# Kernel optimization log

Hardware: AMD Instinct MI355X
Metric: run time of the kernel (lower is better)

The kernel has to match this reference:

```python
import jax, jax.numpy as jnp
import numpy as np
from jax import lax

B, H, W = 256, 28, 28
LATENT = 64
SOM = (16, 16)
FLAT = 7 * 7 * 256  # encoder feature size after two 2x2 pools


def conv2d_same(x, w, b):
    # x: NHWC, w: HWIO
    return lax.conv_general_dilated(x, w, (1, 1), 'SAME',
                                    dimension_numbers=('NHWC', 'HWIO', 'NHWC')) + b


def maxpool_2x2(x):
    return lax.reduce_window(x, -jnp.inf, lax.max, (1, 2, 2, 1), (1, 2, 2, 1), 'SAME')


def upsample_2x(x):
    return jnp.repeat(jnp.repeat(x, 2, axis=1), 2, axis=2)


def encode(x, conv1_w, conv1_b, conv2_w, conv2_b, enc_w, enc_b):
    h = jax.nn.relu(conv2d_same(x, conv1_w, conv1_b))      # [B,28,28,256]
    h = maxpool_2x2(h)                                      # [B,14,14,256]
    h = jax.nn.relu(conv2d_same(h, conv2_w, conv2_b))      # [B,14,14,256]
    h = maxpool_2x2(h)                                      # [B,7,7,256]
    h = h.reshape(h.shape[0], -1)                           # [B,12544]
    return h @ enc_w + enc_b                                # [B,latent]


def decode(z, dec_w, dec_b, deconv1_w, deconv1_b, deconv2_w, deconv2_b):
    h = z @ dec_w + dec_b                                   # [B,12544]
    h = h.reshape(-1, 7, 7, 256)
    h = upsample_2x(h)                                      # [B,14,14,256]
    h = jax.nn.relu(conv2d_same(h, deconv1_w, deconv1_b))
    h = upsample_2x(h)                                      # [B,28,28,256]
    h = conv2d_same(h, deconv2_w, deconv2_b)                # [B,28,28,1]
    return jax.nn.sigmoid(h)


def setup_inputs() -> dict:
    key = jax.random.key(0)
    ks = jax.random.split(key, 12)
    tn = lambda k, shp, s: jax.random.truncated_normal(k, -2.0, 2.0, shp, jnp.float32) * s
    return {
        'x': jax.random.uniform(ks[0], (B, H, W, 1), jnp.float32),
        'conv1_w': tn(ks[1], (4, 4, 1, 256), 0.1),
        'conv1_b': jnp.full((256,), 0.1, jnp.float32),
        'conv2_w': tn(ks[2], (4, 4, 256, 256), 0.1),
        'conv2_b': jnp.full((256,), 0.1, jnp.float32),
        'enc_w': tn(ks[3], (FLAT, LATENT), 0.02),
        'enc_b': jnp.zeros((LATENT,), jnp.float32),
        'embeddings': tn(ks[4], (SOM[0], SOM[1], LATENT), 0.05),
        'dec_w': tn(ks[5], (LATENT, FLAT), 0.02),
        'dec_b': jnp.zeros((FLAT,), jnp.float32),
        'deconv1_w': tn(ks[6], (4, 4, 256, 256), 0.1),
        'deconv1_b': jnp.full((256,), 0.1, jnp.float32),
        'deconv2_w': tn(ks[7], (4, 4, 256, 1), 0.1),
        'deconv2_b': jnp.full((1,), 0.1, jnp.float32),
    }


def reference(x, conv1_w, conv1_b, conv2_w, conv2_b, enc_w, enc_b, embeddings,
              dec_w, dec_b, deconv1_w, deconv1_b, deconv2_w, deconv2_b):
    z_e = encode(x, conv1_w, conv1_b, conv2_w, conv2_b, enc_w, enc_b)  # [B,D]
    emb_flat = embeddings.reshape(-1, LATENT)                          # [K,D]
    # squared euclidean distances [B,K] (cdist pattern)
    z_dist_flat = jnp.sum(jnp.square(z_e[:, None, :] - emb_flat[None, :, :]), axis=-1)
    k = jnp.argmin(z_dist_flat, axis=-1)                               # [B]
    z_q = emb_flat[k]                                                  # [B,D]
    x_hat_e = decode(z_e, dec_w, dec_b, deconv1_w, deconv1_b, deconv2_w, deconv2_b)
    x_hat_q = decode(z_q, dec_w, dec_b, deconv1_w, deconv1_b, deconv2_w, deconv2_b)
    return jnp.stack([x_hat_e, x_hat_q], axis=0)  # [2,B,28,28,1]
```

## Files before the change

### kernel.cpp

```cpp
#include <hip/hip_runtime.h>
#include <hip/hip_bf16.h>

typedef unsigned short u16;
using short8 = __attribute__((ext_vector_type(8))) short;
using half8  = __attribute__((ext_vector_type(8))) _Float16;
using half4  = __attribute__((ext_vector_type(4))) _Float16;
using half2v = __attribute__((ext_vector_type(2))) _Float16;
using f32x4  = __attribute__((ext_vector_type(4))) float;

__device__ __forceinline__ u16 f2bf(float f) {
    unsigned int u = __float_as_uint(f);
    u += 0x7FFFu + ((u >> 16) & 1u);
    return (u16)(u >> 16);
}
__device__ __forceinline__ float bf2f(u16 h) {
    return __uint_as_float(((unsigned int)h) << 16);
}

__device__ __forceinline__ void gl_lds16(const void* g, void* l) {
    __builtin_amdgcn_global_load_lds((const __attribute__((address_space(1))) void*)g,
                                     (__attribute__((address_space(3))) void*)l, 16, 0, 0);
}

__global__ __launch_bounds__(256) void wprep_split_kernel(const float* __restrict__ src,
                                                          u16* __restrict__ hi, u16* __restrict__ lo) {
    int idx = blockIdx.x * 256 + threadIdx.x;
    int ci = idx & 255, n = (idx >> 8) & 255, kk = idx >> 16;
    float v = src[(kk * 256 + ci) * 256 + n];
    u16 h = f2bf(v);
    hi[idx] = h;
    lo[idx] = f2bf(v - bf2f(h));
}

__global__ __launch_bounds__(256) void wprep_f16_kernel(const float* __restrict__ src,
                                                        _Float16* __restrict__ dst) {
    int idx = blockIdx.x * 256 + threadIdx.x;
    int ci = idx & 255, n = (idx >> 8) & 255, kk = idx >> 16;
    dst[idx] = (_Float16)src[(kk * 256 + ci) * 256 + n];
}

__global__ __launch_bounds__(256) void wprep_c2_kernel(const float* __restrict__ src, _Float16* __restrict__ dst) {
    int idx = blockIdx.x * 256 + threadIdx.x;
    dst[idx] = (_Float16)src[idx];
}

__global__ __launch_bounds__(256) void conv1_pool_kernel(const float* __restrict__ x,
                                                         const float* __restrict__ w,
                                                         const float* __restrict__ bias,
                                                         u16* __restrict__ hi, u16* __restrict__ lo) {
    __shared__ float xs[5][5];
    const int blk = blockIdx.x;
    const int px = blk % 14, py = (blk / 14) % 14, b = blk / 196;
    const int t = threadIdx.x;
    if (t < 25) {
        int r = t / 5, c = t % 5;
        int gy = 2 * py - 1 + r, gx = 2 * px - 1 + c;
        xs[r][c] = (gy >= 0 && gy < 28 && gx >= 0 && gx < 28) ? x[(b * 28 + gy) * 28 + gx] : 0.f;
    }
    __syncthreads();
    float wr[16];
#pragma unroll
    for (int k = 0; k < 16; ++k) wr[k] = w[k * 256 + t];
    const float bs = bias[t];
    float m = -1e30f;
#pragma unroll
    for (int dy = 0; dy < 2; ++dy)
#pragma unroll
        for (int dx = 0; dx < 2; ++dx) {
            float acc = bs;
#pragma unroll
            for (int ky = 0; ky < 4; ++ky)
#pragma unroll
                for (int kx = 0; kx < 4; ++kx)
                    acc += xs[dy + ky][dx + kx] * wr[ky * 4 + kx];
            m = fmaxf(m, acc);
        }
    m = fmaxf(m, 0.f);
    u16 h = f2bf(m);
    int o = blk * 256 + t;
    hi[o] = h;
    lo[o] = f2bf(m - bf2f(h));
}

__global__ __launch_bounds__(256, 2) void conv2_split_v2(const u16* __restrict__ Ih, const u16* __restrict__ Il,
                                                         const u16* __restrict__ Wh, const u16* __restrict__ Wl,
                                                         const u16* __restrict__ zg,
                                                         const float* __restrict__ bias, float* __restrict__ out) {
    __shared__ __align__(16) short lds[32768];
    const int AL = 8192, BH = 16384, BL = 24576;
    const int t = threadIdx.x, lane = t & 63, w = t >> 6;
    const int wm = w >> 1, wn = w & 1;
    const int l16 = lane & 15, l4 = lane >> 4;
    const int m0 = blockIdx.x * 128, n0 = blockIdx.y * 128;
    const int rl = lane >> 3;
    const int chS = (((lane & 7) ^ rl)) << 3;
    int ay[4], ax[4], ab[4], wb[4], aoff[4];
    bool av[4];
#pragma unroll
    for (int j = 0; j < 4; ++j) {
        const int r = w * 32 + j * 8 + rl;
        const int gm = m0 + r;
        const int b = gm / 196, rem = gm % 196;
        ay[j] = rem / 14; ax[j] = rem % 14; ab[j] = b * 196;
        wb[j] = (n0 + r) << 8;
    }
    f32x4 acc[4][4] = {};

    for (int kt = 0; kt < 64; ++kt) {
        const int kk = kt >> 2;
        if ((kt & 3) == 0) {
            const int ky = kk >> 2, kx = kk & 3;
#pragma unroll
            for (int j = 0; j < 4; ++j) {
                const int iy = ay[j] + ky - 1, ix = ax[j] + kx - 1;
                av[j] = ((unsigned)iy < 14u) && ((unsigned)ix < 14u);
                aoff[j] = (ab[j] + iy * 14 + ix) << 8;
            }
        }
        const int kc = (kt & 3) << 6;
        __syncthreads();
#pragma unroll
        for (int j = 0; j < 4; ++j) {
            const int rowb = (w * 32 + j * 8) << 6;
            const u16* gh = av[j] ? (Ih + aoff[j] + kc + chS) : zg;
            const u16* gl = av[j] ? (Il + aoff[j] + kc + chS) : zg;
            gl_lds16(gh, lds + rowb);
            gl_lds16(gl, lds + AL + rowb);
            const int woff = (kk << 16) + wb[j] + kc + chS;
            gl_lds16(Wh + woff, lds + BH + rowb);
            gl_lds16(Wl + woff, lds + BL + rowb);
        }
        __syncthreads();
#pragma unroll
        for (int ks = 0; ks < 2; ++ks) {
            short8 bhf[4], blf[4];
#pragma unroll
            for (int ni = 0; ni < 4; ++ni) {
                const int row = wn * 64 + ni * 16 + l16;
                const int p = (ks * 4 + l4) ^ (row & 7);
                const int off = (row << 6) + (p << 3);
                bhf[ni] = *(const short8*)&lds[BH + off];
                blf[ni] = *(const short8*)&lds[BL + off];
            }
#pragma unroll
            for (int mi = 0; mi < 4; ++mi) {
                const int row = wm * 64 + mi * 16 + l16;
                const int p = (ks * 4 + l4) ^ (row & 7);
                const int off = (row << 6) + (p << 3);
                const short8 ah = *(const short8*)&lds[off];
                const short8 al = *(const short8*)&lds[AL + off];
#pragma unroll
                for (int ni = 0; ni < 4; ++ni) {
                    acc[mi][ni] = __builtin_amdgcn_mfma_f32_16x16x32_bf16(ah, bhf[ni], acc[mi][ni], 0, 0, 0);
                    acc[mi][ni] = __builtin_amdgcn_mfma_f32_16x16x32_bf16(ah, blf[ni], acc[mi][ni], 0, 0, 0);
                    acc[mi][ni] = __builtin_amdgcn_mfma_f32_16x16x32_bf16(al, bhf[ni], acc[mi][ni], 0, 0, 0);
                }
            }
        }
    }
#pragma unroll
    for (int ni = 0; ni < 4; ++ni) {
        const int col = n0 + wn * 64 + ni * 16 + l16;
        const float bv = bias[col];
#pragma unroll
        for (int mi = 0; mi < 4; ++mi) {
            const int mrow = m0 + wm * 64 + mi * 16 + l4 * 4;
#pragma unroll
            for (int r = 0; r < 4; ++r)
                out[(size_t)(mrow + r) * 256 + col] = fmaxf(acc[mi][ni][r] + bv, 0.f);
        }
    }
}

__global__ __launch_bounds__(256, 3) void deconv1_f16_v2(const _Float16* __restrict__ I,
                                                         const _Float16* __restrict__ WT,
                                                         const _Float16* __restrict__ zg,
                                                         const float* __restrict__ bias,
                                                         _Float16* __restrict__ out) {
    __shared__ __align__(16) _Float16 lds[16384];
    const int BO = 8192;
    const int t = threadIdx.x, lane = t & 63, w = t >> 6;
    const int wm = w >> 1, wn = w & 1;
    const int l16 = lane & 15, l4 = lane >> 4;
    const int m0 = blockIdx.x * 128, n0 = blockIdx.y * 128;
    const int rl = lane >> 3;
    const int chS = (((lane & 7) ^ rl)) << 3;
    int ay[4], ax[4], ab[4], wb[4], aoff[4];
    bool av[4];
#pragma unroll
    for (int j = 0; j < 4; ++j) {
        const int r = w * 32 + j * 8 + rl;
        const int gm = m0 + r;
        const int b = gm / 196, rem = gm % 196;
        ay[j] = rem / 14; ax[j] = rem % 14; ab[j] = b * 49;
        wb[j] = (n0 + r) << 8;
    }
    f32x4 acc[4][4] = {};

    for (int kt = 0; kt < 64; ++kt) {
        const int kk = kt >> 2;
        if ((kt & 3) == 0) {
            const int ky = kk >> 2, kx = kk & 3;
#pragma unroll
            for (int j = 0; j < 4; ++j) {
                const int iy = ay[j] + ky - 1, ix = ax[j] + kx - 1;
                av[j] = ((unsigned)iy < 14u) && ((unsigned)ix < 14u);
                aoff[j] = (ab[j] + (iy >> 1) * 7 + (ix >> 1)) << 8;
            }
        }
        const int kc = (kt & 3) << 6;
        __syncthreads();
#pragma unroll
        for (int j = 0; j < 4; ++j) {
            const int rowb = (w * 32 + j * 8) << 6;
            const _Float16* ga = av[j] ? (I + aoff[j] + kc + chS) : zg;
            gl_lds16(ga, lds + rowb);
            gl_lds16(WT + (kk << 16) + wb[j] + kc + chS, lds + BO + rowb);
        }
        __syncthreads();
#pragma unroll
        for (int ks = 0; ks < 2; ++ks) {
            half8 bf[4];
#pragma unroll
            for (int ni = 0; ni < 4; ++ni) {
                const int row = wn * 64 + ni * 16 + l16;
                const int p = (ks * 4 + l4) ^ (row & 7);
                bf[ni] = *(const half8*)&lds[BO + (row << 6) + (p << 3)];
            }
#pragma unroll
            for (int mi = 0; mi < 4; ++mi) {
                const int row = wm * 64 + mi * 16 + l16;
                const int p = (ks * 4 + l4) ^ (row & 7);
                const half8 af = *(const half8*)&lds[(row << 6) + (p << 3)];
#pragma unroll
                for (int ni = 0; ni < 4; ++ni)
                    acc[mi][ni] = __builtin_amdgcn_mfma_f32_16x16x32_f16(af, bf[ni], acc[mi][ni], 0, 0, 0);
            }
        }
    }
#pragma unroll
    for (int ni = 0; ni < 4; ++ni) {
        const int col = n0 + wn * 64 + ni * 16 + l16;
        const float bv = bias[col];
#pragma unroll
        for (int mi = 0; mi < 4; ++mi) {
            const int mrow = m0 + wm * 64 + mi * 16 + l4 * 4;
#pragma unroll
            for (int r = 0; r < 4; ++r)
                out[(size_t)(mrow + r) * 256 + col] = (_Float16)fmaxf(acc[mi][ni][r] + bv, 0.f);
        }
    }
}

__global__ __launch_bounds__(256) void pool2_kernel(const float* __restrict__ h2, float* __restrict__ h2p) {
    int idx = blockIdx.x * 256 + threadIdx.x;
    int c = idx & 255;
    int rest = idx >> 8;
    int px = rest % 7, py = (rest / 7) % 7, b = rest / 49;
    const float* base = h2 + (((size_t)(b * 14 + 2 * py)) * 14 + 2 * px) * 256 + c;
    float v = fmaxf(fmaxf(base[0], base[256]), fmaxf(base[14 * 256], base[14 * 256 + 256]));
    h2p[idx] = v;
}

__global__ __launch_bounds__(256) void enc_kernel(const float* __restrict__ h2p, const float* __restrict__ ew,
                                                  const float* __restrict__ eb, float* __restrict__ zcat) {
    __shared__ float arow[12544];
    __shared__ float part[256];
    const int b = blockIdx.x, t = threadIdx.x;
    const float* src = h2p + (size_t)b * 12544;
    for (int i = t; i < 12544; i += 256) arow[i] = src[i];
    __syncthreads();
    const int n = t & 63, chunk = t >> 6;
    float acc = 0.f;
    const int k0 = chunk * 3136;
    for (int k = k0; k < k0 + 3136; ++k) acc += arow[k] * ew[k * 64 + n];
    part[t] = acc;
    __syncthreads();
    if (t < 64) zcat[b * 64 + t] = part[t] + part[t + 64] + part[t + 128] + part[t + 192] + eb[t];
}

__global__ __launch_bounds__(256) void som_kernel(const float* __restrict__ emb, float* __restrict__ zcat) {
    __shared__ float zrow[64];
    __shared__ float sd[256];
    __shared__ int si[256];
    const int b = blockIdx.x, t = threadIdx.x;
    if (t < 64) zrow[t] = zcat[b * 64 + t];
    __syncthreads();
    float acc = 0.f;
    const float* e = emb + t * 64;
    for (int d = 0; d < 64; ++d) { float df = zrow[d] - e[d]; acc += df * df; }
    sd[t] = acc; si[t] = t;
    __syncthreads();
    for (int off = 128; off >= 1; off >>= 1) {
        if (t < off) {
            float d2 = sd[t + off]; int i2 = si[t + off];
            if (d2 < sd[t] || (d2 == sd[t] && i2 < si[t])) { sd[t] = d2; si[t] = i2; }
        }
        __syncthreads();
    }
    const int k = si[0];
    if (t < 64) zcat[(256 + b) * 64 + t] = emb[k * 64 + t];
}

__global__ __launch_bounds__(256) void dec_kernel(const float* __restrict__ zcat, const float* __restrict__ dw,
                                                  const float* __restrict__ db, _Float16* __restrict__ dech) {
    __shared__ float z[8][64];
    const int t = threadIdx.x;
    const int bg = blockIdx.x / 49;
    const int nc = blockIdx.x % 49;
    for (int i = t; i < 512; i += 256) z[i >> 6][i & 63] = zcat[bg * 512 + i];
    __syncthreads();
    const int n = nc * 256 + t;
    const float bv = db[n];
    float acc[8];
#pragma unroll
    for (int j = 0; j < 8; ++j) acc[j] = bv;
    for (int k = 0; k < 64; ++k) {
        float wv = dw[(size_t)k * 12544 + n];
#pragma unroll
        for (int j = 0; j < 8; ++j) acc[j] += z[j][k] * wv;
    }
#pragma unroll
    for (int j = 0; j < 8; ++j) dech[((size_t)(bg * 8 + j)) * 12544 + n] = (_Float16)acc[j];
}

__global__ __launch_bounds__(256) void deconv2_v2(const _Float16* __restrict__ d1, const _Float16* __restrict__ w,
                                                  const float* __restrict__ bias, float* __restrict__ out) {
    __shared__ _Float16 ds[6400];
    __shared__ _Float16 wl[4096];
    const int t = threadIdx.x;
    const int blk = blockIdx.x;
    const int tile = blk % 49, b = blk / 49;
    const int ty = tile / 7, tx = tile % 7;
    const int iy0 = 2 * ty - 1, ix0 = 2 * tx - 1;
    for (int i = t; i < 1024; i += 256)
        *(half4*)&wl[i * 4] = *(const half4*)&w[i * 4];
    const half4 z4 = {};
    for (int i = t; i < 1600; i += 256) {
        const int pix = i >> 6, c4 = (i & 63) << 2;
        const int py = pix / 5, px = pix % 5;
        const int iy = iy0 + py, ix = ix0 + px;
        half4 v = z4;
        if ((unsigned)iy < 14u && (unsigned)ix < 14u)
            v = *(const half4*)&d1[(((size_t)(b * 14 + iy)) * 14 + ix) * 256 + c4];
        *(half4*)&ds[pix * 256 + c4] = v;
    }
    __syncthreads();
    const int wv = t >> 6, lane = t & 63;
    const int ci0 = lane * 4;
    const float bv = bias[0];
#pragma unroll
    for (int pp = 0; pp < 4; ++pp) {
        const int p = wv + pp * 4;
        const int oy = ty * 4 + (p >> 2), ox = tx * 4 + (p & 3);
        float acc = 0.f;
#pragma unroll
        for (int kk = 0; kk < 16; ++kk) {
            const int ky = kk >> 2, kx = kk & 3;
            const int iy = oy + ky - 1, ix = ox + kx - 1;
            if ((unsigned)iy < 28u && (unsigned)ix < 28u) {
                const int lp = ((iy >> 1) - iy0) * 5 + ((ix >> 1) - ix0);
                const half4 dv = *(const half4*)&ds[lp * 256 + ci0];
                const half4 wv4 = *(const half4*)&wl[kk * 256 + ci0];
                half2v dlo = {dv.x, dv.y}, dhi = {dv.z, dv.w};
                half2v wlo = {wv4.x, wv4.y}, whi = {wv4.z, wv4.w};
                acc = __builtin_amdgcn_fdot2(dlo, wlo, acc, false);
                acc = __builtin_amdgcn_fdot2(dhi, whi, acc, false);
            }
        }
#pragma unroll
        for (int off = 32; off; off >>= 1) acc += __shfl_xor(acc, off);
        if (lane == 0) out[(size_t)b * 784 + oy * 28 + ox] = 1.f / (1.f + expf(-(acc + bv)));
    }
}

extern "C" void kernel_launch(void* const* d_in, const int* in_sizes, int n_in,
                              void* d_out, int out_size, void* d_ws, size_t ws_size,
                              hipStream_t stream) {
    const float* x    = (const float*)d_in[0];
    const float* c1w  = (const float*)d_in[1];
    const float* c1b  = (const float*)d_in[2];
    const float* c2w  = (const float*)d_in[3];
    const float* c2b  = (const float*)d_in[4];
    const float* ew   = (const float*)d_in[5];
    const float* eb   = (const float*)d_in[6];
    const float* emb  = (const float*)d_in[7];
    const float* dw   = (const float*)d_in[8];
    const float* db   = (const float*)d_in[9];
    const float* dc1w = (const float*)d_in[10];
    const float* dc1b = (const float*)d_in[11];
    const float* dc2w = (const float*)d_in[12];
    const float* dc2b = (const float*)d_in[13];
    float* out = (float*)d_out;

    char* ws = (char*)d_ws;
    size_t off = 0;
    auto alloc = [&](size_t bytes) { size_t o = off; off += (bytes + 255) & ~(size_t)255; return o; };

    u16*      h1p_hi = (u16*)(ws + alloc((size_t)256 * 196 * 256 * 2));
    u16*      h1p_lo = (u16*)(ws + alloc((size_t)256 * 196 * 256 * 2));
    u16*      w2T_hi = (u16*)(ws + alloc((size_t)16 * 256 * 256 * 2));
    u16*      w2T_lo = (u16*)(ws + alloc((size_t)16 * 256 * 256 * 2));
    float*    h2     = (float*)(ws + alloc((size_t)256 * 196 * 256 * 4));
    float*    h2p    = (float*)(ws + alloc((size_t)256 * 49 * 256 * 4));
    float*    zcat   = (float*)(ws + alloc((size_t)512 * 64 * 4));
    _Float16* dech   = (_Float16*)(ws + alloc((size_t)512 * 49 * 256 * 2));
    _Float16* dw1T   = (_Float16*)(ws + alloc((size_t)16 * 256 * 256 * 2));
    _Float16* d1     = (_Float16*)(ws + alloc((size_t)512 * 196 * 256 * 2));
    _Float16* w2h    = (_Float16*)(ws + alloc((size_t)4096 * 2));
    u16*      zg     = (u16*)(ws + alloc(256));

    hipMemsetAsync(zg, 0, 256, stream);
    wprep_split_kernel<<<4096, 256, 0, stream>>>(c2w, w2T_hi, w2T_lo);
    wprep_f16_kernel<<<4096, 256, 0, stream>>>(dc1w, dw1T);
    wprep_c2_kernel<<<16, 256, 0, stream>>>(dc2w, w2h);
    conv1_pool_kernel<<<50176, 256, 0, stream>>>(x, c1w, c1b, h1p_hi, h1p_lo);
    conv2_split_v2<<<dim3(392, 2), 256, 0, stream>>>(h1p_hi, h1p_lo, w2T_hi, w2T_lo, zg, c2b, h2);
    pool2_kernel<<<12544, 256, 0, stream>>>(h2, h2p);
    enc_kernel<<<256, 256, 0, stream>>>(h2p, ew, eb, zcat);
    som_kernel<<<256, 256, 0, stream>>>(emb, zcat);
    dec_kernel<<<3136, 256, 0, stream>>>(zcat, dw, db, dech);
    deconv1_f16_v2<<<dim3(784, 2), 256, 0, stream>>>(dech, dw1T, (const _Float16*)zg, dc1b, d1);
    deconv2_v2<<<25088, 256, 0, stream>>>(d1, w2h, dc2b, out);
}
```

Before: 891.3 us.

## Polyphase-decompose deconvs, double-buffer conv2 loads, and row-tile conv1

Both deconvolutions that follow nearest-neighbour upsampling are rewritten in polyphase form. The 4x4 taps that read the same source pixel are pre-summed into 9/6/6/4 effective taps per output parity, so deconv1 runs a smaller GEMM directly on the 7x7 input and deconv2 drops to 9 taps per pixel. conv2 gets a double-buffered LDS pipeline using vmcnt waits so global-to-LDS loads overlap the MFMAs. conv1 now handles a whole pooled row per block to cut block count and redundant input loads. Pre-summing the weights in fp16 slightly changes rounding, and the manual waitcnt pipelining depends on the load counts being right.

After: 841.0 us. 1.06x faster.

```diff
diff --git a/kernel.cpp b/kernel.cpp
--- a/kernel.cpp
+++ b/kernel.cpp
@@ -21,6 +21,10 @@
     __builtin_amdgcn_global_load_lds((const __attribute__((address_space(1))) void*)g,
                                      (__attribute__((address_space(3))) void*)l, 16, 0, 0);
 }
+
+#define PIPE_WAIT8() asm volatile("s_waitcnt vmcnt(8)" ::: "memory")
+#define PIPE_WAIT0() asm volatile("s_waitcnt vmcnt(0)" ::: "memory")
+#define BAR() __builtin_amdgcn_s_barrier()
 
 __global__ __launch_bounds__(256) void wprep_split_kernel(const float* __restrict__ src,
                                                           u16* __restrict__ hi, u16* __restrict__ lo) {
@@ -32,132 +36,178 @@
     lo[idx] = f2bf(v - bf2f(h));
 }
 
-__global__ __launch_bounds__(256) void wprep_f16_kernel(const float* __restrict__ src,
-                                                        _Float16* __restrict__ dst) {
-    int idx = blockIdx.x * 256 + threadIdx.x;
-    int ci = idx & 255, n = (idx >> 8) & 255, kk = idx >> 16;
-    dst[idx] = (_Float16)src[(kk * 256 + ci) * 256 + n];
-}
-
-__global__ __launch_bounds__(256) void wprep_c2_kernel(const float* __restrict__ src, _Float16* __restrict__ dst) {
-    int idx = blockIdx.x * 256 + threadIdx.x;
-    dst[idx] = (_Float16)src[idx];
-}
-
-__global__ __launch_bounds__(256) void conv1_pool_kernel(const float* __restrict__ x,
-                                                         const float* __restrict__ w,
-                                                         const float* __restrict__ bias,
-                                                         u16* __restrict__ hi, u16* __restrict__ lo) {
-    __shared__ float xs[5][5];
+__global__ __launch_bounds__(256) void wprep_dc1_par(const float* __restrict__ src, _Float16* __restrict__ dst) {
+    const int idx = blockIdx.x * 256 + threadIdx.x;
+    const int ci = idx & 255, n = (idx >> 8) & 255, tg = idx >> 16;
+    int p, j;
+    if (tg < 9)       { p = 0; j = tg; }
+    else if (tg < 15) { p = 1; j = tg - 9; }
+    else if (tg < 21) { p = 2; j = tg - 15; }
+    else              { p = 3; j = tg - 21; }
+    const int dy = p >> 1, dx = p & 1;
+    const int nx = 3 - dx;
+    const int oyi = j / nx, oxi = j % nx;
+    int ky0, kyn, kx0, kxn;
+    if (dy == 0) { ky0 = (oyi == 0) ? 0 : (oyi == 1 ? 1 : 3); kyn = (oyi == 1) ? 2 : 1; }
+    else         { ky0 = (oyi == 0) ? 0 : 2;                  kyn = 2; }
+    if (dx == 0) { kx0 = (oxi == 0) ? 0 : (oxi == 1 ? 1 : 3); kxn = (oxi == 1) ? 2 : 1; }
+    else         { kx0 = (oxi == 0) ? 0 : 2;                  kxn = 2; }
+    float s = 0.f;
+    for (int a = 0; a < kyn; ++a)
+        for (int c = 0; c < kxn; ++c)
+            s += src[(((ky0 + a) * 4 + (kx0 + c)) * 256 + ci) * 256 + n];
+    dst[((size_t)tg << 16) + (n << 8) + ci] = (_Float16)s;
+}
+
+__global__ __launch_bounds__(256) void wprep_dc2_par(const float* __restrict__ src, _Float16* __restrict__ dst) {
+    const int idx = blockIdx.x * 256 + threadIdx.x;
+    if (idx >= 9216) return;
+    const int ci = idx & 255;
+    const int j9 = (idx >> 8) % 9, p = (idx >> 8) / 9;
+    const int dy = p >> 1, dx = p & 1;
+    const int oyi = j9 / 3, oxi = j9 % 3;
+    float s = 0.f;
+    if (!((dy == 1 && oyi == 2) || (dx == 1 && oxi == 2))) {
+        int ky0, kyn, kx0, kxn;
+        if (dy == 0) { ky0 = (oyi == 0) ? 0 : (oyi == 1 ? 1 : 3); kyn = (oyi == 1) ? 2 : 1; }
+        else         { ky0 = (oyi == 0) ? 0 : 2;                  kyn = 2; }
+        if (dx == 0) { kx0 = (oxi == 0) ? 0 : (oxi == 1 ? 1 : 3); kxn = (oxi == 1) ? 2 : 1; }
+        else         { kx0 = (oxi == 0) ? 0 : 2;                  kxn = 2; }
+        for (int a = 0; a < kyn; ++a)
+            for (int c = 0; c < kxn; ++c)
+                s += src[((ky0 + a) * 4 + (kx0 + c)) * 256 + ci];
+    }
+    dst[idx] = (_Float16)s;
+}
+
+__global__ __launch_bounds__(256) void conv1_pool_v2(const float* __restrict__ x,
+                                                     const float* __restrict__ w,
+                                                     const float* __restrict__ bias,
+                                                     u16* __restrict__ hi, u16* __restrict__ lo) {
+    __shared__ float xs[5][32];
     const int blk = blockIdx.x;
-    const int px = blk % 14, py = (blk / 14) % 14, b = blk / 196;
+    const int py = blk % 14, b = blk / 14;
     const int t = threadIdx.x;
-    if (t < 25) {
-        int r = t / 5, c = t % 5;
-        int gy = 2 * py - 1 + r, gx = 2 * px - 1 + c;
-        xs[r][c] = (gy >= 0 && gy < 28 && gx >= 0 && gx < 28) ? x[(b * 28 + gy) * 28 + gx] : 0.f;
+    for (int i = t; i < 160; i += 256) {
+        const int r = i >> 5, c = i & 31;
+        const int gy = 2 * py - 1 + r, gx = c - 1;
+        float v = 0.f;
+        if ((unsigned)gy < 28u && (unsigned)gx < 28u) v = x[(b * 28 + gy) * 28 + gx];
+        xs[r][c] = v;
     }
     __syncthreads();
     float wr[16];
 #pragma unroll
     for (int k = 0; k < 16; ++k) wr[k] = w[k * 256 + t];
     const float bs = bias[t];
-    float m = -1e30f;
-#pragma unroll
-    for (int dy = 0; dy < 2; ++dy)
-#pragma unroll
-        for (int dx = 0; dx < 2; ++dx) {
-            float acc = bs;
-#pragma unroll
-            for (int ky = 0; ky < 4; ++ky)
-#pragma unroll
-                for (int kx = 0; kx < 4; ++kx)
-                    acc += xs[dy + ky][dx + kx] * wr[ky * 4 + kx];
-            m = fmaxf(m, acc);
-        }
-    m = fmaxf(m, 0.f);
-    u16 h = f2bf(m);
-    int o = blk * 256 + t;
-    hi[o] = h;
-    lo[o] = f2bf(m - bf2f(h));
-}
-
-__global__ __launch_bounds__(256, 2) void conv2_split_v2(const u16* __restrict__ Ih, const u16* __restrict__ Il,
+    for (int px = 0; px < 14; ++px) {
+        float m = 0.f;
+#pragma unroll
+        for (int dy = 0; dy < 2; ++dy)
+#pragma unroll
+            for (int dx = 0; dx < 2; ++dx) {
+                float a = bs;
+#pragma unroll
+                for (int ky = 0; ky < 4; ++ky)
+#pragma unroll
+                    for (int kx = 0; kx < 4; ++kx)
+                        a += xs[dy + ky][2 * px + dx + kx] * wr[ky * 4 + kx];
+                m = fmaxf(m, a);
+            }
+        u16 h = f2bf(m);
+        const int o = ((b * 14 + py) * 14 + px) * 256 + t;
+        hi[o] = h;
+        lo[o] = f2bf(m - bf2f(h));
+    }
+}
+
+__global__ __launch_bounds__(256, 2) void conv2_split_v3(const u16* __restrict__ Ih, const u16* __restrict__ Il,
                                                          const u16* __restrict__ Wh, const u16* __restrict__ Wl,
                                                          const u16* __restrict__ zg,
                                                          const float* __restrict__ bias, float* __restrict__ out) {
     __shared__ __align__(16) short lds[32768];
-    const int AL = 8192, BH = 16384, BL = 24576;
     const int t = threadIdx.x, lane = t & 63, w = t >> 6;
     const int wm = w >> 1, wn = w & 1;
     const int l16 = lane & 15, l4 = lane >> 4;
     const int m0 = blockIdx.x * 128, n0 = blockIdx.y * 128;
-    const int rl = lane >> 3;
-    const int chS = (((lane & 7) ^ rl)) << 3;
-    int ay[4], ax[4], ab[4], wb[4], aoff[4];
-    bool av[4];
+
+    const int rl8 = lane >> 3;
+    const int g = (lane & 7) ^ rl8;
+    const u16* selA = (g < 4 ? Ih : Il) + ((g & 3) << 3);
+    const u16* selB = (g < 4 ? Wh : Wl) + ((g & 3) << 3);
+
+    int ay[4], ax[4], ab[4], wb[4];
 #pragma unroll
     for (int j = 0; j < 4; ++j) {
-        const int r = w * 32 + j * 8 + rl;
+        const int r = w * 32 + j * 8 + rl8;
         const int gm = m0 + r;
         const int b = gm / 196, rem = gm % 196;
         ay[j] = rem / 14; ax[j] = rem % 14; ab[j] = b * 196;
         wb[j] = (n0 + r) << 8;
     }
+    int aoff[4]; bool av[4];
+    auto dectap = [&](int kk) {
+        const int ky = kk >> 2, kx = kk & 3;
+#pragma unroll
+        for (int j = 0; j < 4; ++j) {
+            const int iy = ay[j] + ky - 1, ix = ax[j] + kx - 1;
+            av[j] = ((unsigned)iy < 14u) && ((unsigned)ix < 14u);
+            aoff[j] = (ab[j] + iy * 14 + ix) << 8;
+        }
+    };
+    int rdA[4], rdB[4];
+#pragma unroll
+    for (int mi = 0; mi < 4; ++mi) {
+        const int ra = wm * 64 + mi * 16 + l16;
+        rdA[mi] = (ra << 6) + ((l4 ^ (ra & 7)) << 3);
+    }
+#pragma unroll
+    for (int ni = 0; ni < 4; ++ni) {
+        const int rb = wn * 64 + ni * 16 + l16;
+        rdB[ni] = 8192 + (rb << 6) + ((l4 ^ (rb & 7)) << 3);
+    }
+    auto stage = [&](int h) {
+        const int kk = h >> 3, kc = (h & 7) << 5;
+        const int buf = (h & 1) << 14;
+#pragma unroll
+        for (int j = 0; j < 4; ++j) {
+            const int rowb = buf + ((w * 32 + j * 8) << 6);
+            const u16* asrc = av[j] ? (selA + aoff[j] + kc) : zg;
+            gl_lds16(asrc, lds + rowb);
+            gl_lds16(selB + (kk << 16) + wb[j] + kc, lds + 8192 + rowb);
+        }
+    };
+
     f32x4 acc[4][4] = {};
-
-    for (int kt = 0; kt < 64; ++kt) {
-        const int kk = kt >> 2;
-        if ((kt & 3) == 0) {
-            const int ky = kk >> 2, kx = kk & 3;
-#pragma unroll
-            for (int j = 0; j < 4; ++j) {
-                const int iy = ay[j] + ky - 1, ix = ax[j] + kx - 1;
-                av[j] = ((unsigned)iy < 14u) && ((unsigned)ix < 14u);
-                aoff[j] = (ab[j] + iy * 14 + ix) << 8;
+    dectap(0);
+    stage(0);
+    for (int h = 0; h < 128; ++h) {
+        const int hn = (h < 127) ? h + 1 : 127;
+        if ((hn & 7) == 0) dectap(hn >> 3);
+        stage(hn);
+        PIPE_WAIT8();
+        BAR();
+        const int base = (h & 1) << 14;
+        short8 bh8[4], bl8[4];
+#pragma unroll
+        for (int ni = 0; ni < 4; ++ni) {
+            bh8[ni] = *(const short8*)&lds[base + rdB[ni]];
+            bl8[ni] = *(const short8*)&lds[base + (rdB[ni] ^ 32)];
+        }
+#pragma unroll
+        for (int mi = 0; mi < 4; ++mi) {
+            const short8 ah = *(const short8*)&lds[base + rdA[mi]];
+            const short8 al = *(const short8*)&lds[base + (rdA[mi] ^ 32)];
+#pragma unroll
+            for (int ni = 0; ni < 4; ++ni) {
+                acc[mi][ni] = __builtin_amdgcn_mfma_f32_16x16x32_bf16(ah, bh8[ni], acc[mi][ni], 0, 0, 0);
+                acc[mi][ni] = __builtin_amdgcn_mfma_f32_16x16x32_bf16(ah, bl8[ni], acc[mi][ni], 0, 0, 0);
+                acc[mi][ni] = __builtin_amdgcn_mfma_f32_16x16x32_bf16(al, bh8[ni], acc[mi][ni], 0, 0, 0);
             }
         }
-        const int kc = (kt & 3) << 6;
-        __syncthreads();
-#pragma unroll
-        for (int j = 0; j < 4; ++j) {
-            const int rowb = (w * 32 + j * 8) << 6;
-            const u16* gh = av[j] ? (Ih + aoff[j] + kc + chS) : zg;
-            const u16* gl = av[j] ? (Il + aoff[j] + kc + chS) : zg;
-            gl_lds16(gh, lds + rowb);
-            gl_lds16(gl, lds + AL + rowb);
-            const int woff = (kk << 16) + wb[j] + kc + chS;
-            gl_lds16(Wh + woff, lds + BH + rowb);
-            gl_lds16(Wl + woff, lds + BL + rowb);
-        }
-        __syncthreads();
-#pragma unroll
-        for (int ks = 0; ks < 2; ++ks) {
-            short8 bhf[4], blf[4];
-#pragma unroll
-            for (int ni = 0; ni < 4; ++ni) {
-                const int row = wn * 64 + ni * 16 + l16;
-                const int p = (ks * 4 + l4) ^ (row & 7);
-                const int off = (row << 6) + (p << 3);
-                bhf[ni] = *(const short8*)&lds[BH + off];
-                blf[ni] = *(const short8*)&lds[BL + off];
-            }
-#pragma unroll
-            for (int mi = 0; mi < 4; ++mi) {
-                const int row = wm * 64 + mi * 16 + l16;
-                const int p = (ks * 4 + l4) ^ (row & 7);
-                const int off = (row << 6) + (p << 3);
-                const short8 ah = *(const short8*)&lds[off];
-                const short8 al = *(const short8*)&lds[AL + off];
-#pragma unroll
-                for (int ni = 0; ni < 4; ++ni) {
-                    acc[mi][ni] = __builtin_amdgcn_mfma_f32_16x16x32_bf16(ah, bhf[ni], acc[mi][ni], 0, 0, 0);
-                    acc[mi][ni] = __builtin_amdgcn_mfma_f32_16x16x32_bf16(ah, blf[ni], acc[mi][ni], 0, 0, 0);
-                    acc[mi][ni] = __builtin_amdgcn_mfma_f32_16x16x32_bf16(al, bhf[ni], acc[mi][ni], 0, 0, 0);
-                }
-            }
-        }
-    }
+        BAR();
+    }
+    PIPE_WAIT0();
 #pragma unroll
     for (int ni = 0; ni < 4; ++ni) {
         const int col = n0 + wn * 64 + ni * 16 + l16;
@@ -172,82 +222,112 @@
     }
 }
 
-__global__ __launch_bounds__(256, 3) void deconv1_f16_v2(const _Float16* __restrict__ I,
-                                                         const _Float16* __restrict__ WT,
-                                                         const _Float16* __restrict__ zg,
-                                                         const float* __restrict__ bias,
-                                                         _Float16* __restrict__ out) {
-    __shared__ __align__(16) _Float16 lds[16384];
-    const int BO = 8192;
+__global__ __launch_bounds__(256, 2) void deconv1_par(const _Float16* __restrict__ I,
+                                                      const _Float16* __restrict__ WC,
+                                                      const _Float16* __restrict__ zg,
+                                                      const float* __restrict__ bias,
+                                                      _Float16* __restrict__ out) {
+    __shared__ __align__(16) _Float16 lds[32768];
     const int t = threadIdx.x, lane = t & 63, w = t >> 6;
     const int wm = w >> 1, wn = w & 1;
     const int l16 = lane & 15, l4 = lane >> 4;
     const int m0 = blockIdx.x * 128, n0 = blockIdx.y * 128;
-    const int rl = lane >> 3;
-    const int chS = (((lane & 7) ^ rl)) << 3;
-    int ay[4], ax[4], ab[4], wb[4], aoff[4];
-    bool av[4];
+    const int p = blockIdx.z, dy = p >> 1, dx = p & 1;
+    const int nx = 3 - dx;
+    const int ntaps = (3 - dy) * nx;
+    const int pbase = (dy == 0) ? (dx == 0 ? 0 : 9) : (dx == 0 ? 15 : 21);
+    const int nkt = ntaps * 4;
+
+    const int rl8 = lane >> 3;
+    const int g = (lane & 7) ^ rl8;
+    const _Float16* selA = I + (g << 3);
+    const _Float16* selB = WC + ((size_t)pbase << 16) + (g << 3);
+
+    int aY[4], aX[4], ab[4], wb[4];
 #pragma unroll
     for (int j = 0; j < 4; ++j) {
-        const int r = w * 32 + j * 8 + rl;
+        const int r = w * 32 + j * 8 + rl8;
         const int gm = m0 + r;
-        const int b = gm / 196, rem = gm % 196;
-        ay[j] = rem / 14; ax[j] = rem % 14; ab[j] = b * 49;
+        const int b = gm / 49, rem = gm % 49;
+        aY[j] = rem / 7; aX[j] = rem % 7; ab[j] = b * 49;
         wb[j] = (n0 + r) << 8;
     }
+    int aoff[4]; bool av[4];
+    auto dectap = [&](int kk) {
+        const int oy = kk / nx - (dy == 0 ? 1 : 0);
+        const int ox = kk % nx - (dx == 0 ? 1 : 0);
+#pragma unroll
+        for (int j = 0; j < 4; ++j) {
+            const int iy = aY[j] + oy, ix = aX[j] + ox;
+            av[j] = ((unsigned)iy < 7u) && ((unsigned)ix < 7u);
+            aoff[j] = (ab[j] + iy * 7 + ix) << 8;
+        }
+    };
+    int rdA[4], rdB[4];
+#pragma unroll
+    for (int mi = 0; mi < 4; ++mi) {
+        const int ra = wm * 64 + mi * 16 + l16;
+        rdA[mi] = (ra << 6) + ((l4 ^ (ra & 7)) << 3);
+    }
+#pragma unroll
+    for (int ni = 0; ni < 4; ++ni) {
+        const int rb = wn * 64 + ni * 16 + l16;
+        rdB[ni] = 8192 + (rb << 6) + ((l4 ^ (rb & 7)) << 3);
+    }
+    auto stage = [&](int kt) {
+        const int kk = kt >> 2, kc = (kt & 3) << 6;
+        const int buf = (kt & 1) << 14;
+#pragma unroll
+        for (int j = 0; j < 4; ++j) {
+            const int rowb = buf + ((w * 32 + j * 8) << 6);
+            const _Float16* asrc = av[j] ? (selA + aoff[j] + kc) : zg;
+            gl_lds16(asrc, lds + rowb);
+            gl_lds16(selB + (kk << 16) + wb[j] + kc, lds + 8192 + rowb);
+        }
+    };
+
     f32x4 acc[4][4] = {};
-
-    for (int kt = 0; kt < 64; ++kt) {
-        const int kk = kt >> 2;
-        if ((kt & 3) == 0) {
-            const int ky = kk >> 2, kx = kk & 3;
-#pragma unroll
-            for (int j = 0; j < 4; ++j) {
-                const int iy = ay[j] + ky - 1, ix = ax[j] + kx - 1;
-                av[j] = ((unsigned)iy < 14u) && ((unsigned)ix < 14u);
-                aoff[j] = (ab[j] + (iy >> 1) * 7 + (ix >> 1)) << 8;
+    dectap(0);
+    stage(0);
+    for (int kt = 0; kt < nkt; ++kt) {
+        const int ktn = (kt < nkt - 1) ? kt + 1 : kt;
+        if ((ktn & 3) == 0 && ktn == kt + 1) dectap(ktn >> 2);
+        stage(ktn);
+        PIPE_WAIT8();
+        BAR();
+        const int base = (kt & 1) << 14;
+#pragma unroll
+        for (int ks = 0; ks < 2; ++ks) {
+            const int x32 = ks << 5;
+            half8 b8[4];
+#pragma unroll
+            for (int ni = 0; ni < 4; ++ni)
+                b8[ni] = *(const half8*)&lds[base + (rdB[ni] ^ x32)];
+#pragma unroll
+            for (int mi = 0; mi < 4; ++mi) {
+                const half8 a8 = *(const half8*)&lds[base + (rdA[mi] ^ x32)];
+#pragma unroll
+                for (int ni = 0; ni < 4; ++ni)
+                    acc[mi][ni] = __builtin_amdgcn_mfma_f32_16x16x32_f16(a8, b8[ni], acc[mi][ni], 0, 0, 0);
             }
         }
-        const int kc = (kt & 3) << 6;
-        __syncthreads();
-#pragma unroll
-        for (int j = 0; j < 4; ++j) {
-            const int rowb = (w * 32 + j * 8) << 6;
-            const _Float16* ga = av[j] ? (I + aoff[j] + kc + chS) : zg;
-            gl_lds16(ga, lds + rowb);
-            gl_lds16(WT + (kk << 16) + wb[j] + kc + chS, lds + BO + rowb);
-        }
-        __syncthreads();
-#pragma unroll
-        for (int ks = 0; ks < 2; ++ks) {
-            half8 bf[4];
+        BAR();
+    }
+    PIPE_WAIT0();
+#pragma unroll
+    for (int mi = 0; mi < 4; ++mi) {
+        const int mb = m0 + wm * 64 + mi * 16 + l4 * 4;
+#pragma unroll
+        for (int r = 0; r < 4; ++r) {
+            const int m = mb + r;
+            const int b = m / 49, rem = m % 49;
+            const int Y = rem / 7, X = rem % 7;
+            _Float16* op = out + (((size_t)(b * 196 + (2 * Y + dy) * 14 + (2 * X + dx))) << 8);
 #pragma unroll
             for (int ni = 0; ni < 4; ++ni) {
-                const int row = wn * 64 + ni * 16 + l16;
-                const int p = (ks * 4 + l4) ^ (row & 7);
-                bf[ni] = *(const half8*)&lds[BO + (row << 6) + (p << 3)];
+                const int col = n0 + wn * 64 + ni * 16 + l16;
+                op[col] = (_Float16)fmaxf(acc[mi][ni][r] + bias[col], 0.f);
             }
-#pragma unroll
-            for (int mi = 0; mi < 4; ++mi) {
-                const int row = wm * 64 + mi * 16 + l16;
-                const int p = (ks * 4 + l4) ^ (row & 7);
-                const half8 af = *(const half8*)&lds[(row << 6) + (p << 3)];
-#pragma unroll
-                for (int ni = 0; ni < 4; ++ni)
-                    acc[mi][ni] = __builtin_amdgcn_mfma_f32_16x16x32_f16(af, bf[ni], acc[mi][ni], 0, 0, 0);
-            }
-        }
-    }
-#pragma unroll
-    for (int ni = 0; ni < 4; ++ni) {
-        const int col = n0 + wn * 64 + ni * 16 + l16;
-        const float bv = bias[col];
-#pragma unroll
-        for (int mi = 0; mi < 4; ++mi) {
-            const int mrow = m0 + wm * 64 + mi * 16 + l4 * 4;
-#pragma unroll
-            for (int r = 0; r < 4; ++r)
-                out[(size_t)(mrow + r) * 256 + col] = (_Float16)fmaxf(acc[mi][ni][r] + bv, 0.f);
         }
     }
 }
@@ -324,17 +404,17 @@
     for (int j = 0; j < 8; ++j) dech[((size_t)(bg * 8 + j)) * 12544 + n] = (_Float16)acc[j];
 }
 
-__global__ __launch_bounds__(256) void deconv2_v2(const _Float16* __restrict__ d1, const _Float16* __restrict__ w,
+__global__ __launch_bounds__(256) void deconv2_v3(const _Float16* __restrict__ d1, const _Float16* __restrict__ w2c,
                                                   const float* __restrict__ bias, float* __restrict__ out) {
     __shared__ _Float16 ds[6400];
-    __shared__ _Float16 wl[4096];
+    __shared__ _Float16 wl[9216];
     const int t = threadIdx.x;
     const int blk = blockIdx.x;
     const int tile = blk % 49, b = blk / 49;
     const int ty = tile / 7, tx = tile % 7;
     const int iy0 = 2 * ty - 1, ix0 = 2 * tx - 1;
-    for (int i = t; i < 1024; i += 256)
-        *(half4*)&wl[i * 4] = *(const half4*)&w[i * 4];
+    for (int i = t; i < 2304; i += 256)
+        *(half4*)&wl[i * 4] = *(const half4*)&w2c[i * 4];
     const half4 z4 = {};
     for (int i = t; i < 1600; i += 256) {
         const int pix = i >> 6, c4 = (i & 63) << 2;
@@ -351,22 +431,24 @@
     const float bv = bias[0];
 #pragma unroll
     for (int pp = 0; pp < 4; ++pp) {
-        const int p = wv + pp * 4;
-        const int oy = ty * 4 + (p >> 2), ox = tx * 4 + (p & 3);
+        const int pq = wv + pp * 4;
+        const int oy = ty * 4 + (pq >> 2), ox = tx * 4 + (pq & 3);
+        const int dy = oy & 1, Y = oy >> 1;
+        const int dxp = ox & 1, X = ox >> 1;
+        const _Float16* wbase = wl + ((dy * 2 + dxp) * 9) * 256 + ci0;
         float acc = 0.f;
 #pragma unroll
-        for (int kk = 0; kk < 16; ++kk) {
-            const int ky = kk >> 2, kx = kk & 3;
-            const int iy = oy + ky - 1, ix = ox + kx - 1;
-            if ((unsigned)iy < 28u && (unsigned)ix < 28u) {
-                const int lp = ((iy >> 1) - iy0) * 5 + ((ix >> 1) - ix0);
-                const half4 dv = *(const half4*)&ds[lp * 256 + ci0];
-                const half4 wv4 = *(const half4*)&wl[kk * 256 + ci0];
-                half2v dlo = {dv.x, dv.y}, dhi = {dv.z, dv.w};
-                half2v wlo = {wv4.x, wv4.y}, whi = {wv4.z, wv4.w};
-                acc = __builtin_amdgcn_fdot2(dlo, wlo, acc, false);
-                acc = __builtin_amdgcn_fdot2(dhi, whi, acc, false);
-            }
+        for (int j = 0; j < 9; ++j) {
+            const int oyi = j / 3, oxi = j % 3;
+            const int iy = Y + oyi - (dy == 0 ? 1 : 0);
+            const int ix = X + oxi - (dxp == 0 ? 1 : 0);
+            const int lp = (iy - iy0) * 5 + (ix - ix0);
+            const half4 dv = *(const half4*)&ds[lp * 256 + ci0];
+            const half4 wv4 = *(const half4*)&wbase[j * 256];
+            half2v dlo = {dv.x, dv.y}, dhi = {dv.z, dv.w};
+            half2v wlo = {wv4.x, wv4.y}, whi = {wv4.z, wv4.w};
+            acc = __builtin_amdgcn_fdot2(dlo, wlo, acc, false);
+            acc = __builtin_amdgcn_fdot2(dhi, whi, acc, false);
         }
 #pragma unroll
         for (int off = 32; off; off >>= 1) acc += __shfl_xor(acc, off);
@@ -405,21 +487,21 @@
     float*    h2p    = (float*)(ws + alloc((size_t)256 * 49 * 256 * 4));
     float*    zcat   = (float*)(ws + alloc((size_t)512 * 64 * 4));
     _Float16* dech   = (_Float16*)(ws + alloc((size_t)512 * 49 * 256 * 2));
-    _Float16* dw1T   = (_Float16*)(ws + alloc((size_t)16 * 256 * 256 * 2));
+    _Float16* wc1    = (_Float16*)(ws + alloc((size_t)25 * 256 * 256 * 2));
     _Float16* d1     = (_Float16*)(ws + alloc((size_t)512 * 196 * 256 * 2));
-    _Float16* w2h    = (_Float16*)(ws + alloc((size_t)4096 * 2));
+    _Float16* w2c    = (_Float16*)(ws + alloc((size_t)9216 * 2));
     u16*      zg     = (u16*)(ws + alloc(256));
 
     hipMemsetAsync(zg, 0, 256, stream);
     wprep_split_kernel<<<4096, 256, 0, stream>>>(c2w, w2T_hi, w2T_lo);
-    wprep_f16_kernel<<<4096, 256, 0, stream>>>(dc1w, dw1T);
-    wprep_c2_kernel<<<16, 256, 0, stream>>>(dc2w, w2h);
-    conv1_pool_kernel<<<50176, 256, 0, stream>>>(x, c1w, c1b, h1p_hi, h1p_lo);
-    conv2_split_v2<<<dim3(392, 2), 256, 0, stream>>>(h1p_hi, h1p_lo, w2T_hi, w2T_lo, zg, c2b, h2);
+    wprep_dc1_par<<<6400, 256, 0, stream>>>(dc1w, wc1);
+    wprep_dc2_par<<<36, 256, 0, stream>>>(dc2w, w2c);
+    conv1_pool_v2<<<3584, 256, 0, stream>>>(x, c1w, c1b, h1p_hi, h1p_lo);
+    conv2_split_v3<<<dim3(392, 2), 256, 0, stream>>>(h1p_hi, h1p_lo, w2T_hi, w2T_lo, zg, c2b, h2);
     pool2_kernel<<<12544, 256, 0, stream>>>(h2, h2p);
     enc_kernel<<<256, 256, 0, stream>>>(h2p, ew, eb, zcat);
     som_kernel<<<256, 256, 0, stream>>>(emb, zcat);
     dec_kernel<<<3136, 256, 0, stream>>>(zcat, dw, db, dech);
-    deconv1_f16_v2<<<dim3(784, 2), 256, 0, stream>>>(dech, dw1T, (const _Float16*)zg, dc1b, d1);
-    deconv2_v2<<<25088, 256, 0, stream>>>(d1, w2h, dc2b, out);
-}
+    deconv1_par<<<dim3(196, 2, 4), 256, 0, stream>>>(dech, wc1, (const _Float16*)zg, dc1b, d1);
+    deconv2_v3<<<25088, 256, 0, stream>>>(d1, w2c, dc2b, out);
+}
```
